# Kernel tuning notes

Hardware: AMD Instinct MI355X
Metric: run time of the kernel (lower is better)

## Reference

```python
import jax, jax.numpy as jnp
import numpy as np

NEG = -1e9

def _lstm(x, Wih, Whh, b):
    # x: [B,S,D]; PyTorch gate order i,f,g,o; Wih:[4H,D], Whh:[4H,H], b:[4H]
    B = x.shape[0]
    H = Whh.shape[1]
    def step(carry, xt):
        h, c = carry
        g = xt @ Wih.T + h @ Whh.T + b
        i, f, gg, o = jnp.split(g, 4, axis=-1)
        c = jax.nn.sigmoid(f) * c + jax.nn.sigmoid(i) * jnp.tanh(gg)
        h = jax.nn.sigmoid(o) * jnp.tanh(c)
        return (h, c), h
    init = (jnp.zeros((B, H), x.dtype), jnp.zeros((B, H), x.dtype))
    _, hs = jax.lax.scan(step, init, x.transpose(1, 0, 2))
    return hs.transpose(1, 0, 2)  # [B,S,H]

def _bilstm(x, Wih_f, Whh_f, b_f, Wih_b, Whh_b, b_b):
    fwd = _lstm(x, Wih_f, Whh_f, b_f)
    bwd = jnp.flip(_lstm(jnp.flip(x, 1), Wih_b, Whh_b, b_b), 1)
    return jnp.concatenate([fwd, bwd], axis=-1)

def _windowed_attention(h, attn_W, attn_b, window_size):
    # score(i,j) = W @ [h_i, h_j, h_i*h_j] + b, decomposed exactly:
    #   = h_i@w1 + h_j@w2 + (h_i*w3)@h_j + b, masked to |i-j| <= window
    S = h.shape[1]
    w1, w2, w3 = jnp.split(attn_W[0], 3)
    s1 = h @ w1                                   # [B,S]
    s2 = h @ w2                                   # [B,S]
    cross = jnp.einsum('bid,bjd->bij', h * w3, h)  # [B,S,S]
    scores = s1[:, :, None] + s2[:, None, :] + cross + attn_b[0]
    idx = jnp.arange(S)
    band = jnp.abs(idx[:, None] - idx[None, :]) <= window_size
    scores = jnp.where(band, scores, NEG)
    p = jax.nn.softmax(scores, axis=-1)
    return jnp.einsum('bij,bjd->bid', p, h)       # [B,S,H]

def _forward(x, lstm1_Wih_f, lstm1_Whh_f, lstm1_b_f, lstm1_Wih_b, lstm1_Whh_b, lstm1_b_b,
             fc1_W, fc1_b, attn_W, attn_b,
             lstm2_Wih_f, lstm2_Whh_f, lstm2_b_f, lstm2_Wih_b, lstm2_Whh_b, lstm2_b_b,
             l2_W1, l2_b1, l2_W2, l2_b2, l2_W3, l2_b3, window_size):
    # dropout layers are identity at inference
    lstm_out = _bilstm(x, lstm1_Wih_f, lstm1_Whh_f, lstm1_b_f,
                       lstm1_Wih_b, lstm1_Whh_b, lstm1_b_b)          # [B,S,768]
    h = lstm_out @ fc1_W.T + fc1_b                                    # [B,S,384]
    attn = _windowed_attention(h, attn_W, attn_b, window_size)        # [B,S,384]
    h_cat = jnp.concatenate([h, attn], axis=-1)                       # [B,S,768]
    lstm_out2 = _bilstm(h_cat, lstm2_Wih_f, lstm2_Whh_f, lstm2_b_f,
                        lstm2_Wih_b, lstm2_Whh_b, lstm2_b_b)          # [B,S,768]
    h2 = lstm_out2 @ fc1_W.T + fc1_b                                  # fc1 reused, as in source
    y = jax.nn.relu(h2 @ l2_W1.T + l2_b1)
    y = jax.nn.relu(y @ l2_W2.T + l2_b2)
    return y @ l2_W3.T + l2_b3                                        # [B,S,1]

def setup_inputs() -> dict:
    key = jax.random.key(0)
    ks = iter(jax.random.split(key, 32))
    D, H, B, S = 768, 384, 16, 1024
    sc = 0.02
    def rn(shape):
        return jax.random.normal(next(ks), shape, dtype=jnp.float32) * sc
    inp = {'x': jax.random.normal(next(ks), (B, S, D), dtype=jnp.float32)}
    for name in ('lstm1', 'lstm2'):
        inp[f'{name}_Wih_f'] = rn((4 * H, D)); inp[f'{name}_Whh_f'] = rn((4 * H, H))
        inp[f'{name}_b_f'] = rn((4 * H,))
        inp[f'{name}_Wih_b'] = rn((4 * H, D)); inp[f'{name}_Whh_b'] = rn((4 * H, H))
        inp[f'{name}_b_b'] = rn((4 * H,))
    inp['fc1_W'] = rn((H, D)); inp['fc1_b'] = rn((H,))
    inp['attn_W'] = rn((1, 3 * H)); inp['attn_b'] = rn((1,))
    inp['l2_W1'] = rn((256, H)); inp['l2_b1'] = rn((256,))
    inp['l2_W2'] = rn((96, 256)); inp['l2_b2'] = rn((96,))
    inp['l2_W3'] = rn((1, 96)); inp['l2_b3'] = rn((1,))
    inp['window_size'] = 32
    return inp

def reference(x, lstm1_Wih_f, lstm1_Whh_f, lstm1_b_f, lstm1_Wih_b, lstm1_Whh_b, lstm1_b_b,
              fc1_W, fc1_b, attn_W, attn_b,
              lstm2_Wih_f, lstm2_Whh_f, lstm2_b_f, lstm2_Wih_b, lstm2_Whh_b, lstm2_b_b,
              l2_W1, l2_b1, l2_W2, l2_b2, l2_W3, l2_b3, window_size):
    return _forward(x, lstm1_Wih_f, lstm1_Whh_f, lstm1_b_f, lstm1_Wih_b, lstm1_Whh_b, lstm1_b_b,
                    fc1_W, fc1_b, attn_W, attn_b,
                    lstm2_Wih_f, lstm2_Whh_f, lstm2_b_f, lstm2_Wih_b, lstm2_Whh_b, lstm2_b_b,
                    l2_W1, l2_b1, l2_W2, l2_b2, l2_W3, l2_b3, window_size)
```

## Files before the change

### kernel.cpp

```cpp
#include <hip/hip_runtime.h>
#include <hip/hip_bf16.h>
#include <type_traits>

#define S_LEN 1024
#define BATCH 16
#define HID   384
#define DIN   768

#define GRP 8
#define UPB 48
#define NTHR 384

__device__ __forceinline__ float sigf(float x)     { return 1.f/(1.f + __expf(-x)); }
__device__ __forceinline__ float tanhfast(float x) { return 1.f - 2.f/(__expf(2.f*x) + 1.f); }

__global__ void zero_kernel(unsigned long long* hx)
{
    int i = blockIdx.x * blockDim.x + threadIdx.x;
    if (i < 32*2*HID) hx[i] = 0ull;
}

template<int RELU, typename OT>
__global__ __launch_bounds__(256) void gemm_nt(
    const float* __restrict__ A, int ldA,
    const float* __restrict__ W,
    const float* __restrict__ bias,
    OT* __restrict__ C, int ldC,
    int M, int N, int K)
{
    __shared__ float As[16][132];
    __shared__ float Ws[16][68];
    const int tid = threadIdx.x;
    const int m0 = blockIdx.x * 128;
    const int n0 = blockIdx.y * 64;
    const int tm = (tid & 15) * 8;
    const int tn = (tid >> 4) * 4;

    float acc[8][4];
    #pragma unroll
    for (int i = 0; i < 8; i++)
        #pragma unroll
        for (int j = 0; j < 4; j++) acc[i][j] = 0.f;

    const int lrow = tid >> 2;
    const int lk   = (tid & 3) * 4;

    for (int k0 = 0; k0 < K; k0 += 16) {
        #pragma unroll
        for (int p = 0; p < 2; p++) {
            const int r = lrow + p * 64;
            const float4 av = *(const float4*)(A + (size_t)(m0 + r) * ldA + k0 + lk);
            As[lk+0][r] = av.x; As[lk+1][r] = av.y; As[lk+2][r] = av.z; As[lk+3][r] = av.w;
        }
        {
            float4 wv = make_float4(0.f, 0.f, 0.f, 0.f);
            if (n0 + lrow < N) wv = *(const float4*)(W + (size_t)(n0 + lrow) * K + k0 + lk);
            Ws[lk+0][lrow] = wv.x; Ws[lk+1][lrow] = wv.y; Ws[lk+2][lrow] = wv.z; Ws[lk+3][lrow] = wv.w;
        }
        __syncthreads();
        #pragma unroll
        for (int k = 0; k < 16; k++) {
            const float4 a0 = *(const float4*)&As[k][tm];
            const float4 a1 = *(const float4*)&As[k][tm + 4];
            const float4 bv = *(const float4*)&Ws[k][tn];
            const float am[8] = {a0.x, a0.y, a0.z, a0.w, a1.x, a1.y, a1.z, a1.w};
            const float bb[4] = {bv.x, bv.y, bv.z, bv.w};
            #pragma unroll
            for (int i = 0; i < 8; i++)
                #pragma unroll
                for (int j = 0; j < 4; j++) acc[i][j] += am[i] * bb[j];
        }
        __syncthreads();
    }

    #pragma unroll
    for (int i = 0; i < 8; i++) {
        const int m = m0 + tm + i;
        #pragma unroll
        for (int j = 0; j < 4; j++) {
            const int n = n0 + tn + j;
            if (n < N) {
                float v = acc[i][j] + bias[n];
                if (RELU) v = fmaxf(v, 0.f);
                if constexpr (std::is_same_v<OT, __hip_bfloat16>)
                    C[(size_t)m * ldC + n] = __float2bfloat16(v);
                else
                    C[(size_t)m * ldC + n] = v;
            }
        }
    }
}

__global__ __launch_bounds__(NTHR) void lstm_scan(
    const __hip_bfloat16* __restrict__ gatesF, const __hip_bfloat16* __restrict__ gatesB,
    const float* __restrict__ WhhF,            const float* __restrict__ WhhB,
    float* __restrict__ out, unsigned long long* hx_all, int epoch)
{
    __shared__ float hl[2][HID];

    const int blk = blockIdx.x;
    const int g   = blk & 31;
    const int m   = blk >> 5;
    const int dir = g >> 4;
    const int b   = g & 15;
    const int u0  = m * UPB;

    const __hip_bfloat16* gates = dir ? gatesB : gatesF;
    const float* Whh = dir ? WhhB : WhhF;
    unsigned long long* hx = hx_all + g * (2 * HID);

    const int tid = threadIdx.x;
    const int rr  = tid >> 3;
    const int ss  = tid & 7;
    const int ug  = u0 + rr;
    const bool owner = (ss == 0);

    float w[4][UPB];
    #pragma unroll
    for (int gt = 0; gt < 4; gt++) {
        const float* wp = Whh + ((size_t)gt * HID + ug) * HID + ss * 4;
        #pragma unroll
        for (int j = 0; j < 12; j++) {
            const float4 v = *(const float4*)(wp + 32 * j);
            w[gt][4*j+0] = v.x; w[gt][4*j+1] = v.y;
            w[gt][4*j+2] = v.z; w[gt][4*j+3] = v.w;
        }
    }

    float c_state = 0.f;
    const unsigned tbase = (unsigned)epoch * 2048u;

    for (int t = 0; t < S_LEN; t++) {
        const int tt = dir ? (S_LEN - 1 - t) : t;

        float gx0 = 0.f, gx1 = 0.f, gx2 = 0.f, gx3 = 0.f;
        if (owner) {
            const __hip_bfloat16* gp = gates + ((size_t)(b * S_LEN + tt)) * (4 * HID) + ug;
            gx0 = __bfloat162float(gp[0]);
            gx1 = __bfloat162float(gp[HID]);
            gx2 = __bfloat162float(gp[2 * HID]);
            gx3 = __bfloat162float(gp[3 * HID]);
        }

        if (t == 0) {
            if (tid < 128) {
                hl[0][tid] = 0.f; hl[0][tid + 128] = 0.f; hl[0][tid + 256] = 0.f;
            }
        } else if (tid < 128) {
            const unsigned long long* src = hx + ((t + 1) & 1) * HID;
            float* dst = hl[t & 1];
            const unsigned tgt = tbase + (unsigned)t;
            int pend = 7;
            long guard = 0;
            do {
                if (pend & 1) {
                    const unsigned long long q = __hip_atomic_load(src + tid,
                        __ATOMIC_RELAXED, __HIP_MEMORY_SCOPE_AGENT);
                    if ((unsigned)(q >> 32) >= tgt) {
                        dst[tid] = __uint_as_float((unsigned)q); pend &= ~1;
                    }
                }
                if (pend & 2) {
                    const unsigned long long q = __hip_atomic_load(src + tid + 128,
                        __ATOMIC_RELAXED, __HIP_MEMORY_SCOPE_AGENT);
                    if ((unsigned)(q >> 32) >= tgt) {
                        dst[tid + 128] = __uint_as_float((unsigned)q); pend &= ~2;
                    }
                }
                if (pend & 4) {
                    const unsigned long long q = __hip_atomic_load(src + tid + 256,
                        __ATOMIC_RELAXED, __HIP_MEMORY_SCOPE_AGENT);
                    if ((unsigned)(q >> 32) >= tgt) {
                        dst[tid + 256] = __uint_as_float((unsigned)q); pend &= ~4;
                    }
                }
                if (!pend) break;
                __builtin_amdgcn_s_sleep(1);
            } while (++guard < (1L << 22));
        }
        __syncthreads();

        const float* hsl = hl[t & 1];
        float a0 = 0.f, a1 = 0.f, a2 = 0.f, a3 = 0.f;
        #pragma unroll
        for (int j = 0; j < 12; j++) {
            const float4 h4 = *(const float4*)(hsl + ss * 4 + 32 * j);
            const float hh[4] = {h4.x, h4.y, h4.z, h4.w};
            #pragma unroll
            for (int e = 0; e < 4; e++) {
                a0 += w[0][4*j+e] * hh[e];
                a1 += w[1][4*j+e] * hh[e];
                a2 += w[2][4*j+e] * hh[e];
                a3 += w[3][4*j+e] * hh[e];
            }
        }
        a0 += __shfl_xor(a0, 1, 64); a0 += __shfl_xor(a0, 2, 64); a0 += __shfl_xor(a0, 4, 64);
        a1 += __shfl_xor(a1, 1, 64); a1 += __shfl_xor(a1, 2, 64); a1 += __shfl_xor(a1, 4, 64);
        a2 += __shfl_xor(a2, 1, 64); a2 += __shfl_xor(a2, 2, 64); a2 += __shfl_xor(a2, 4, 64);
        a3 += __shfl_xor(a3, 1, 64); a3 += __shfl_xor(a3, 2, 64); a3 += __shfl_xor(a3, 4, 64);

        if (owner) {
            const float ii = sigf(a0 + gx0);
            const float ff = sigf(a1 + gx1);
            const float gg = tanhfast(a2 + gx2);
            const float oo = sigf(a3 + gx3);
            c_state = ff * c_state + ii * gg;
            const float hn = oo * tanhfast(c_state);
            const unsigned long long pk =
                ((unsigned long long)(tbase + (unsigned)t + 1u) << 32) |
                (unsigned long long)__float_as_uint(hn);
            __hip_atomic_store(hx + (t & 1) * HID + ug, pk,
                               __ATOMIC_RELAXED, __HIP_MEMORY_SCOPE_AGENT);
            out[((size_t)(b * S_LEN + tt)) * (2 * HID) + dir * HID + ug] = hn;
        }
    }
}

__global__ __launch_bounds__(256) void attn_win(
    const float* __restrict__ hcat,
    const float* __restrict__ attnW,
    float* __restrict__ ocat,
    const int* __restrict__ wsz_p)
{
    __shared__ float q[HID];
    __shared__ float sc[96];
    __shared__ float p[96];
    const int blk = blockIdx.x;
    const int b = blk >> 10, i = blk & 1023;
    const int W = *wsz_p;
    const int jlo = max(i - W, 0), jhi = min(i + W, S_LEN - 1);
    const int nj = jhi - jlo + 1;
    const int tid = threadIdx.x;
    const float* hrow = hcat + (size_t)b * S_LEN * 768;

    if (tid < 96) {
        const float4 hv = *(const float4*)(hrow + (size_t)i * 768 + tid * 4);
        const float4 w3 = *(const float4*)(attnW + 768 + tid * 4);
        const float4 w2 = *(const float4*)(attnW + 384 + tid * 4);
        float4 r;
        r.x = hv.x*w3.x + w2.x; r.y = hv.y*w3.y + w2.y;
        r.z = hv.z*w3.z + w2.z; r.w = hv.w*w3.w + w2.w;
        *(float4*)(q + tid * 4) = r;
    }
    __syncthreads();

    const int wv = tid >> 6, lane = tid & 63;
    for (int jj = wv; jj < nj; jj += 4) {
        const float* hj = hrow + (size_t)(jlo + jj) * 768;
        float s = 0.f;
        #pragma unroll
        for (int c = 0; c < 6; c++) { const int d = lane + 64*c; s += q[d] * hj[d]; }
        #pragma unroll
        for (int st = 1; st < 64; st <<= 1) s += __shfl_xor(s, st, 64);
        if (lane == 0) sc[jj] = s;
    }
    __syncthreads();

    if (tid < 64) {
        float v1 = (tid < nj) ? sc[tid] : -3e38f;
        float v2 = (64 + tid < nj) ? sc[64 + tid] : -3e38f;
        float m = fmaxf(v1, v2);
        #pragma unroll
        for (int st = 1; st < 64; st <<= 1) m = fmaxf(m, __shfl_xor(m, st, 64));
        float e1 = (tid < nj) ? __expf(v1 - m) : 0.f;
        float e2 = (64 + tid < nj) ? __expf(v2 - m) : 0.f;
        float sum = e1 + e2;
        #pragma unroll
        for (int st = 1; st < 64; st <<= 1) sum += __shfl_xor(sum, st, 64);
        const float inv = 1.f / sum;
        if (tid < nj) p[tid] = e1 * inv;
        if (64 + tid < nj) p[64 + tid] = e2 * inv;
    }
    __syncthreads();

    if (tid < 192) {
        const int d = tid * 2;
        float s0 = 0.f, s1 = 0.f;
        for (int jj = 0; jj < nj; jj++) {
            const float* hj = hrow + (size_t)(jlo + jj) * 768 + d;
            const float pj = p[jj];
            s0 += pj * hj[0]; s1 += pj * hj[1];
        }
        float* o = ocat + (size_t)b * S_LEN * 768 + (size_t)i * 768 + 384 + d;
        o[0] = s0; o[1] = s1;
    }
}

__global__ __launch_bounds__(256) void final_dot(
    const float* __restrict__ y2, const float* __restrict__ W3,
    const float* __restrict__ b3, float* __restrict__ outp)
{
    __shared__ float w[96];
    const int tid = threadIdx.x;
    if (tid < 96) w[tid] = W3[tid];
    __syncthreads();
    const int r = blockIdx.x * 256 + tid;
    const float* row = y2 + (size_t)r * 96;
    float s = 0.f;
    #pragma unroll
    for (int c = 0; c < 24; c++) {
        const float4 v = ((const float4*)row)[c];
        s += v.x*w[c*4] + v.y*w[c*4+1] + v.z*w[c*4+2] + v.w*w[c*4+3];
    }
    outp[r] = s + b3[0];
}

extern "C" void kernel_launch(void* const* d_in, const int* in_sizes, int n_in,
                              void* d_out, int out_size, void* d_ws, size_t ws_size,
                              hipStream_t stream)
{
    const float* x        = (const float*)d_in[0];
    const float* l1_Wih_f = (const float*)d_in[1];
    const float* l1_Whh_f = (const float*)d_in[2];
    const float* l1_b_f   = (const float*)d_in[3];
    const float* l1_Wih_b = (const float*)d_in[4];
    const float* l1_Whh_b = (const float*)d_in[5];
    const float* l1_b_b   = (const float*)d_in[6];
    const float* l2_Wih_f = (const float*)d_in[7];
    const float* l2_Whh_f = (const float*)d_in[8];
    const float* l2_b_f   = (const float*)d_in[9];
    const float* l2_Wih_b = (const float*)d_in[10];
    const float* l2_Whh_b = (const float*)d_in[11];
    const float* l2_b_b   = (const float*)d_in[12];
    const float* fc1_W    = (const float*)d_in[13];
    const float* fc1_b    = (const float*)d_in[14];
    const float* attn_W   = (const float*)d_in[15];
    const float* w1       = (const float*)d_in[17];
    const float* b1       = (const float*)d_in[18];
    const float* w2       = (const float*)d_in[19];
    const float* b2       = (const float*)d_in[20];
    const float* w3       = (const float*)d_in[21];
    const float* b3       = (const float*)d_in[22];
    const int*   wsz      = (const int*)d_in[23];

    char* wsb = (char*)d_ws;
    __hip_bfloat16*     gF  = (__hip_bfloat16*)(wsb);
    __hip_bfloat16*     gB  = (__hip_bfloat16*)(wsb +  50331648);
    float*              seq = (float*)(wsb + 100663296);
    float*              hct = (float*)(wsb + 150994944);
    unsigned long long* hx  = (unsigned long long*)(wsb + 201326592);
    float*              h2  = (float*)(wsb);
    float*              y1  = (float*)(wsb +  50331648);
    float*              y2  = (float*)(wsb +  50331648 + 16777216);

    const int M = BATCH * S_LEN;
    dim3 tb(256);

    zero_kernel<<<dim3(96), tb, 0, stream>>>(hx);
    gemm_nt<0, __hip_bfloat16><<<dim3(M/128, 24), tb, 0, stream>>>(x, DIN, l1_Wih_f, l1_b_f, gF, 1536, M, 1536, DIN);
    gemm_nt<0, __hip_bfloat16><<<dim3(M/128, 24), tb, 0, stream>>>(x, DIN, l1_Wih_b, l1_b_b, gB, 1536, M, 1536, DIN);
    lstm_scan<<<dim3(256), dim3(NTHR), 0, stream>>>(gF, gB, l1_Whh_f, l1_Whh_b, seq, hx, 0);

    gemm_nt<0, float><<<dim3(M/128, 6), tb, 0, stream>>>(seq, 768, fc1_W, fc1_b, hct, 768, M, 384, 768);
    attn_win<<<dim3(M), tb, 0, stream>>>(hct, attn_W, hct, wsz);

    gemm_nt<0, __hip_bfloat16><<<dim3(M/128, 24), tb, 0, stream>>>(hct, 768, l2_Wih_f, l2_b_f, gF, 1536, M, 1536, 768);
    gemm_nt<0, __hip_bfloat16><<<dim3(M/128, 24), tb, 0, stream>>>(hct, 768, l2_Wih_b, l2_b_b, gB, 1536, M, 1536, 768);
    lstm_scan<<<dim3(256), dim3(NTHR), 0, stream>>>(gF, gB, l2_Whh_f, l2_Whh_b, seq, hx, 1);

    gemm_nt<0, float><<<dim3(M/128, 6), tb, 0, stream>>>(seq, 768, fc1_W, fc1_b, h2, 384, M, 384, 768);
    gemm_nt<1, float><<<dim3(M/128, 4), tb, 0, stream>>>(h2, 384, w1, b1, y1, 256, M, 256, 384);
    gemm_nt<1, float><<<dim3(M/128, 2), tb, 0, stream>>>(y1, 256, w2, b2, y2, 96, M, 96, 256);
    final_dot<<<dim3(M/256), tb, 0, stream>>>(y2, w3, b3, (float*)d_out);
}
```

Measured before the change: 7.108 ms.

## Batch four sequences per LSTM block and stream recurrent weights from cache

Reworks the persistent LSTM scan so each block processes four batch rows over 12 hidden units, rather than one batch row over 48 units, which cuts the number of cooperating groups from 32 to 8 per layer. Recurrent weights are no longer held in registers and are reloaded with float4 global loads every timestep, relying on L1/L2 to keep them close. This raises weight reuse across batch rows and lowers register pressure, at the cost of global weight traffic in the serial loop. The host-side grid size and launch code are not visible and must match the new layout.

```diff
diff --git a/kernel.cpp b/kernel.cpp
--- a/kernel.cpp
+++ b/kernel.cpp
@@ -7,8 +7,10 @@
 #define HID   384
 #define DIN   768
 
-#define GRP 8
-#define UPB 48
+#define NGRP 8
+#define GRP  32
+#define BQ   4
+#define UPB  12
 #define NTHR 384
 
 __device__ __forceinline__ float sigf(float x)     { return 1.f/(1.f + __expf(-x)); }
@@ -17,7 +19,7 @@
 __global__ void zero_kernel(unsigned long long* hx)
 {
     int i = blockIdx.x * blockDim.x + threadIdx.x;
-    if (i < 32*2*HID) hx[i] = 0ull;
+    if (i < 24576) hx[i] = 0ull;
 }
 
 template<int RELU, typename OT>
@@ -96,36 +98,30 @@
     const float* __restrict__ WhhF,            const float* __restrict__ WhhB,
     float* __restrict__ out, unsigned long long* hx_all, int epoch)
 {
-    __shared__ float hl[2][HID];
+    __shared__ float hl[2][BQ * HID];
 
     const int blk = blockIdx.x;
-    const int g   = blk & 31;
-    const int m   = blk >> 5;
-    const int dir = g >> 4;
-    const int b   = g & 15;
+    const int g   = blk & 7;
+    const int m   = blk >> 3;
+    const int dir = g >> 2;
+    const int b0  = (g & 3) * BQ;
     const int u0  = m * UPB;
 
     const __hip_bfloat16* gates = dir ? gatesB : gatesF;
     const float* Whh = dir ? WhhB : WhhF;
-    unsigned long long* hx = hx_all + g * (2 * HID);
+    unsigned long long* hx = hx_all + g * (2 * BQ * HID);
 
     const int tid = threadIdx.x;
-    const int rr  = tid >> 3;
-    const int ss  = tid & 7;
+    const int bb  = tid & 3;
+    const int ss  = (tid >> 2) & 7;
+    const int rr  = tid >> 5;
     const int ug  = u0 + rr;
     const bool owner = (ss == 0);
 
-    float w[4][UPB];
-    #pragma unroll
-    for (int gt = 0; gt < 4; gt++) {
-        const float* wp = Whh + ((size_t)gt * HID + ug) * HID + ss * 4;
-        #pragma unroll
-        for (int j = 0; j < 12; j++) {
-            const float4 v = *(const float4*)(wp + 32 * j);
-            w[gt][4*j+0] = v.x; w[gt][4*j+1] = v.y;
-            w[gt][4*j+2] = v.z; w[gt][4*j+3] = v.w;
-        }
-    }
+    const float* wp0 = Whh + ((size_t)0 * HID + ug) * HID + ss * 4;
+    const float* wp1 = Whh + ((size_t)1 * HID + ug) * HID + ss * 4;
+    const float* wp2 = Whh + ((size_t)2 * HID + ug) * HID + ss * 4;
+    const float* wp3 = Whh + ((size_t)3 * HID + ug) * HID + ss * 4;
 
     float c_state = 0.f;
     const unsigned tbase = (unsigned)epoch * 2048u;
@@ -135,7 +131,8 @@
 
         float gx0 = 0.f, gx1 = 0.f, gx2 = 0.f, gx3 = 0.f;
         if (owner) {
-            const __hip_bfloat16* gp = gates + ((size_t)(b * S_LEN + tt)) * (4 * HID) + ug;
+            const __hip_bfloat16* gp =
+                gates + ((size_t)((b0 + bb) * S_LEN + tt)) * (4 * HID) + ug;
             gx0 = __bfloat162float(gp[0]);
             gx1 = __bfloat162float(gp[HID]);
             gx2 = __bfloat162float(gp[2 * HID]);
@@ -143,35 +140,24 @@
         }
 
         if (t == 0) {
-            if (tid < 128) {
-                hl[0][tid] = 0.f; hl[0][tid + 128] = 0.f; hl[0][tid + 256] = 0.f;
-            }
-        } else if (tid < 128) {
-            const unsigned long long* src = hx + ((t + 1) & 1) * HID;
+            hl[0][tid] = 0.f; hl[0][tid + 384] = 0.f;
+            hl[0][tid + 768] = 0.f; hl[0][tid + 1152] = 0.f;
+        } else {
+            const unsigned long long* src = hx + ((t + 1) & 1) * (BQ * HID);
             float* dst = hl[t & 1];
             const unsigned tgt = tbase + (unsigned)t;
-            int pend = 7;
+            int pend = 15;
             long guard = 0;
             do {
-                if (pend & 1) {
-                    const unsigned long long q = __hip_atomic_load(src + tid,
-                        __ATOMIC_RELAXED, __HIP_MEMORY_SCOPE_AGENT);
-                    if ((unsigned)(q >> 32) >= tgt) {
-                        dst[tid] = __uint_as_float((unsigned)q); pend &= ~1;
-                    }
-                }
-                if (pend & 2) {
-                    const unsigned long long q = __hip_atomic_load(src + tid + 128,
-                        __ATOMIC_RELAXED, __HIP_MEMORY_SCOPE_AGENT);
-                    if ((unsigned)(q >> 32) >= tgt) {
-                        dst[tid + 128] = __uint_as_float((unsigned)q); pend &= ~2;
-                    }
-                }
-                if (pend & 4) {
-                    const unsigned long long q = __hip_atomic_load(src + tid + 256,
-                        __ATOMIC_RELAXED, __HIP_MEMORY_SCOPE_AGENT);
-                    if ((unsigned)(q >> 32) >= tgt) {
-                        dst[tid + 256] = __uint_as_float((unsigned)q); pend &= ~4;
+                #pragma unroll
+                for (int p = 0; p < 4; p++) {
+                    if (pend & (1 << p)) {
+                        const unsigned long long q = __hip_atomic_load(src + tid + 384 * p,
+                            __ATOMIC_RELAXED, __HIP_MEMORY_SCOPE_AGENT);
+                        if ((unsigned)(q >> 32) >= tgt) {
+                            dst[tid + 384 * p] = __uint_as_float((unsigned)q);
+                            pend &= ~(1 << p);
+                        }
                     }
                 }
                 if (!pend) break;
@@ -180,24 +166,24 @@
         }
         __syncthreads();
 
-        const float* hsl = hl[t & 1];
+        const float* hrow = hl[t & 1] + bb * HID;
         float a0 = 0.f, a1 = 0.f, a2 = 0.f, a3 = 0.f;
         #pragma unroll
         for (int j = 0; j < 12; j++) {
-            const float4 h4 = *(const float4*)(hsl + ss * 4 + 32 * j);
-            const float hh[4] = {h4.x, h4.y, h4.z, h4.w};
-            #pragma unroll
-            for (int e = 0; e < 4; e++) {
-                a0 += w[0][4*j+e] * hh[e];
-                a1 += w[1][4*j+e] * hh[e];
-                a2 += w[2][4*j+e] * hh[e];
-                a3 += w[3][4*j+e] * hh[e];
-            }
-        }
-        a0 += __shfl_xor(a0, 1, 64); a0 += __shfl_xor(a0, 2, 64); a0 += __shfl_xor(a0, 4, 64);
-        a1 += __shfl_xor(a1, 1, 64); a1 += __shfl_xor(a1, 2, 64); a1 += __shfl_xor(a1, 4, 64);
-        a2 += __shfl_xor(a2, 1, 64); a2 += __shfl_xor(a2, 2, 64); a2 += __shfl_xor(a2, 4, 64);
-        a3 += __shfl_xor(a3, 1, 64); a3 += __shfl_xor(a3, 2, 64); a3 += __shfl_xor(a3, 4, 64);
+            const float4 h4 = *(const float4*)(hrow + ss * 4 + 32 * j);
+            const float4 w0 = *(const float4*)(wp0 + 32 * j);
+            const float4 w1 = *(const float4*)(wp1 + 32 * j);
+            const float4 w2 = *(const float4*)(wp2 + 32 * j);
+            const float4 w3 = *(const float4*)(wp3 + 32 * j);
+            a0 += h4.x*w0.x + h4.y*w0.y + h4.z*w0.z + h4.w*w0.w;
+            a1 += h4.x*w1.x + h4.y*w1.y + h4.z*w1.z + h4.w*w1.w;
+            a2 += h4.x*w2.x + h4.y*w2.y + h4.z*w2.z + h4.w*w2.w;
+            a3 += h4.x*w3.x + h4.y*w3.y + h4.z*w3.z + h4.w*w3.w;
+        }
+        a0 += __shfl_xor(a0, 4, 64); a0 += __shfl_xor(a0, 8, 64); a0 += __shfl_xor(a0, 16, 64);
+        a1 += __shfl_xor(a1, 4, 64); a1 += __shfl_xor(a1, 8, 64); a1 += __shfl_xor(a1, 16, 64);
+        a2 += __shfl_xor(a2, 4, 64); a2 += __shfl_xor(a2, 8, 64); a2 += __shfl_xor(a2, 16, 64);
+        a3 += __shfl_xor(a3, 4, 64); a3 += __shfl_xor(a3, 8, 64); a3 += __shfl_xor(a3, 16, 64);
 
         if (owner) {
             const float ii = sigf(a0 + gx0);
@@ -209,9 +195,9 @@
             const unsigned long long pk =
                 ((unsigned long long)(tbase + (unsigned)t + 1u) << 32) |
                 (unsigned long long)__float_as_uint(hn);
-            __hip_atomic_store(hx + (t & 1) * HID + ug, pk,
+            __hip_atomic_store(hx + (t & 1) * (BQ * HID) + bb * HID + ug, pk,
                                __ATOMIC_RELAXED, __HIP_MEMORY_SCOPE_AGENT);
-            out[((size_t)(b * S_LEN + tt)) * (2 * HID) + dir * HID + ug] = hn;
+            out[((size_t)((b0 + bb) * S_LEN + tt)) * (2 * HID) + dir * HID + ug] = hn;
         }
     }
 }
```

Result: slower. 8.422 ms (+18.5%).
